# Kernel tuning notes

Measured on AMD Instinct MI355X. Metric: run time of the kernel, lower is better.

Reference implementation:

```python
import jax, jax.numpy as jnp
import numpy as np

T, HID, H, KV, D = 2048, 2048, 16, 8, 128
EPS = 1e-6
THETA = 10000.0


def setup_inputs() -> dict:
    key = jax.random.key(0)
    ks = jax.random.split(key, 4)
    return {
        "positions": jnp.arange(T, dtype=jnp.int32),
        "hidden_states": jax.random.normal(ks[0], (T, HID), dtype=jnp.float32),
        "layernorm_weight": jnp.ones((HID,), dtype=jnp.float32),
        "qkv_weight": jax.random.normal(ks[1], ((H + 2 * KV) * D, HID), dtype=jnp.float32) * 0.02,
        "q_norm_weight": jnp.ones((D,), dtype=jnp.float32),
        "k_norm_weight": jnp.ones((D,), dtype=jnp.float32),
        "o_weight": jax.random.normal(ks[2], (HID, H * D), dtype=jnp.float32) * 0.02,
    }


def _rms(x, w, eps=EPS):
    var = jnp.mean(jnp.square(x), axis=-1, keepdims=True)
    return x * jax.lax.rsqrt(var + eps) * w


def _rope(x, pos):
    # NeoX-style rotary over full head_dim. x: [T, nH, D]
    inv_freq = 1.0 / (THETA ** (jnp.arange(0, D, 2, dtype=jnp.float32) / D))
    ang = pos.astype(jnp.float32)[:, None] * inv_freq  # [T, D/2]
    cos, sin = jnp.cos(ang)[:, None, :], jnp.sin(ang)[:, None, :]
    x1, x2 = x[..., : D // 2], x[..., D // 2 :]
    return jnp.concatenate([x1 * cos - x2 * sin, x2 * cos + x1 * sin], axis=-1)


def reference(positions, hidden_states, layernorm_weight, qkv_weight,
              q_norm_weight, k_norm_weight, o_weight):
    # Fused RMSNorm + QKV projection
    normed = _rms(hidden_states, layernorm_weight)                 # [T, HID]
    qkv = normed @ qkv_weight.T                                    # [T, (H+2KV)*D]
    q, k, v = jnp.split(qkv, [H * D, (H + KV) * D], axis=-1)
    q = _rms(q.reshape(T, H, D), q_norm_weight)                    # per-head q norm
    k = _rms(k.reshape(T, KV, D), k_norm_weight)                   # per-head k norm
    v = v.reshape(T, KV, D)
    # RoPE
    q = _rope(q, positions)
    k = _rope(k, positions)
    # GQA causal attention
    scale = D ** -0.5
    kr = jnp.repeat(k, H // KV, axis=1)                            # [T, H, D]
    vr = jnp.repeat(v, H // KV, axis=1)
    scores = jnp.einsum("qhd,khd->hqk", q, kr) * scale             # [H, T, T]
    mask = jnp.tril(jnp.ones((T, T), dtype=bool))
    scores = jnp.where(mask[None], scores, jnp.finfo(scores.dtype).min)
    attn = jax.nn.softmax(scores, axis=-1)
    out = jnp.einsum("hqk,khd->qhd", attn, vr).reshape(T, H * D)
    return out @ o_weight.T                                        # [T, HID]
```

## Files before the change

kernel.cpp:

```cpp
#include <hip/hip_runtime.h>
#include <cstdint>
#include <cstddef>

typedef __bf16 bf16;
typedef __attribute__((ext_vector_type(8))) __bf16 bf16x8;
typedef __attribute__((ext_vector_type(4))) __bf16 bf16x4v;
typedef __attribute__((ext_vector_type(4))) float f32x4;
typedef __attribute__((ext_vector_type(16))) float f32x16;
typedef __attribute__((ext_vector_type(4))) short short4v;

#define T_N   2048
#define HID_N 2048
#define NH    16
#define NKV   8
#define HD    128

#define MFMA(a, b, c)   __builtin_amdgcn_mfma_f32_16x16x32_bf16((a), (b), (c), 0, 0, 0)
#define MFMA32(a, b, c) __builtin_amdgcn_mfma_f32_32x32x16_bf16((a), (b), (c), 0, 0, 0)

__device__ __forceinline__ f32x4 MFMA16(short4v a, short4v b, f32x4 c) {
#if __has_builtin(__builtin_amdgcn_mfma_f32_16x16x16bf16_1k)
    return __builtin_amdgcn_mfma_f32_16x16x16bf16_1k(a, b, c, 0, 0, 0);
#else
    asm volatile("v_mfma_f32_16x16x16_bf16 %0, %1, %2, %0\n\ts_nop 7\n\ts_nop 7"
                 : "+v"(c) : "v"(a), "v"(b));
    return c;
#endif
}

__device__ __forceinline__ void gl_lds16(const void* g, void* l) {
    __builtin_amdgcn_global_load_lds(
        (const __attribute__((address_space(1))) unsigned int*)g,
        (__attribute__((address_space(3))) unsigned int*)l,
        16, 0, 0);
}

__device__ __forceinline__ uint32_t pk2(float a, float b) {
    union { bf16 h; unsigned short u; } ca, cb;
    ca.h = (bf16)a; cb.h = (bf16)b;
    return ((uint32_t)cb.u << 16) | ca.u;
}

__device__ __forceinline__ void y2cq(int y, int& ci, int& qt) {
    if (y < 25)       { ci = 0; qt = y + 7; }
    else if (y < 42)  { ci = 1; qt = y - 10; }
    else if (y < 51)  { ci = 2; qt = y - 19; }
    else if (y == 51) { ci = 3; qt = 31; }
    else { int z = y - 52; int k = 7 - (z >> 2); ci = z & 3; qt = 8 * ci + k - 1; }
}
__device__ __forceinline__ int yof(int ci, int qt) {
    int k = qt + 1 - 8 * ci;
    if (k >= 8) {
        if (ci == 0) return qt - 7;
        if (ci == 1) return qt + 10;
        if (ci == 2) return qt + 19;
        return 51;
    }
    return 52 + (7 - k) * 4 + ci;
}

__global__ __launch_bounds__(256) void k_pre(const float* __restrict__ qkvw,
                                             bf16* __restrict__ qkvw_b,
                                             const float* __restrict__ ow,
                                             bf16* __restrict__ ow_b,
                                             const float* __restrict__ hid,
                                             const float* __restrict__ lw,
                                             bf16* __restrict__ normed,
                                             const int* __restrict__ pos,
                                             float2* __restrict__ rope) {
    const int blk = blockIdx.x, tid = threadIdx.x;
    if (blk < 6144) {
        const float* src; bf16* dst;
        if (blk < 4096) { int i = blk * 2048 + tid * 8; src = qkvw + i; dst = qkvw_b + i; }
        else            { int i = (blk - 4096) * 2048 + tid * 8; src = ow + i; dst = ow_b + i; }
        float4 x = ((const float4*)src)[0], y = ((const float4*)src)[1];
        bf16x8 v;
        v[0] = (bf16)x.x; v[1] = (bf16)x.y; v[2] = (bf16)x.z; v[3] = (bf16)x.w;
        v[4] = (bf16)y.x; v[5] = (bf16)y.y; v[6] = (bf16)y.z; v[7] = (bf16)y.w;
        *(bf16x8*)dst = v;
        return;
    }
    if (blk >= 8192) {
        const int t = (blk - 8192) * 4 + (tid >> 6);
        const int j = tid & 63;
        float ang = (float)pos[t] * __powf(10000.f, -(float)j * (1.f / 64.f));
        float s, c;
        __sincosf(ang, &s, &c);
        rope[t * 64 + j] = make_float2(c, s);
        return;
    }
    const int row = blk - 6144;
    const float* xr = hid + (size_t)row * HID_N;
    float4 a = ((const float4*)xr)[tid * 2];
    float4 b = ((const float4*)xr)[tid * 2 + 1];
    float ss = a.x*a.x + a.y*a.y + a.z*a.z + a.w*a.w
             + b.x*b.x + b.y*b.y + b.z*b.z + b.w*b.w;
    #pragma unroll
    for (int m = 32; m; m >>= 1) ss += __shfl_xor(ss, m);
    __shared__ float red[4];
    if ((tid & 63) == 0) red[tid >> 6] = ss;
    __syncthreads();
    float tot = red[0] + red[1] + red[2] + red[3];
    float rs = rsqrtf(tot * (1.0f / HID_N) + 1e-6f);
    const float4* wr = (const float4*)(lw + tid * 8);
    float4 wa = wr[0], wb = wr[1];
    bf16x8 v;
    v[0] = (bf16)(a.x * rs * wa.x); v[1] = (bf16)(a.y * rs * wa.y);
    v[2] = (bf16)(a.z * rs * wa.z); v[3] = (bf16)(a.w * rs * wa.w);
    v[4] = (bf16)(b.x * rs * wb.x); v[5] = (bf16)(b.y * rs * wb.y);
    v[6] = (bf16)(b.z * rs * wb.z); v[7] = (bf16)(b.w * rs * wb.w);
    *(bf16x8*)(normed + (size_t)row * HID_N + tid * 8) = v;
}

__global__ __launch_bounds__(256, 3) void k_gemm_qkv(const bf16* __restrict__ A,
                                                     const bf16* __restrict__ B,
                                                     bf16* __restrict__ qkv3,
                                                     bf16* __restrict__ vb) {
    const int K = HID_N;
    __shared__ __attribute__((aligned(16))) bf16 As[128 * 64];
    __shared__ __attribute__((aligned(16))) bf16 Bs[128 * 64];
    const int tid = threadIdx.x;
    const int lane = tid & 63, wid = tid >> 6;
    const int wm = wid >> 1, wn = wid & 1;
    const int col31 = lane & 31, khalf = lane >> 5;
    const int orig = blockIdx.y * gridDim.x + blockIdx.x;
    const int wgid = (orig & 7) * 64 + (orig >> 3);
    const size_t bm = (size_t)(wgid >> 5) * 128, bn = (size_t)(wgid & 31) * 128;

    f32x16 acc[2][2] = {};
    const int srow = tid >> 3;
    const int schk = tid & 7;

    for (int k0 = 0; k0 < K; k0 += 64) {
        __syncthreads();
        #pragma unroll
        for (int c = 0; c < 4; c++) {
            int row = c * 32 + srow;
            int ka = (schk ^ (row & 7)) << 3;
            gl_lds16(A + (bm + row) * (size_t)K + k0 + ka,
                     (char*)As + c * 4096 + tid * 16);
            gl_lds16(B + (bn + row) * (size_t)K + k0 + ka,
                     (char*)Bs + c * 4096 + tid * 16);
        }
        __syncthreads();
        #pragma unroll
        for (int kb = 0; kb < 4; kb++) {
            bf16x8 af[2], bfr[2];
            #pragma unroll
            for (int mt = 0; mt < 2; mt++) {
                int row = wm * 64 + mt * 32 + col31;
                af[mt] = *(const bf16x8*)(As + row * 64 + (((2 * kb + khalf) ^ (row & 7)) << 3));
            }
            #pragma unroll
            for (int nt = 0; nt < 2; nt++) {
                int row = wn * 64 + nt * 32 + col31;
                bfr[nt] = *(const bf16x8*)(Bs + row * 64 + (((2 * kb + khalf) ^ (row & 7)) << 3));
            }
            #pragma unroll
            for (int mt = 0; mt < 2; mt++)
                #pragma unroll
                for (int nt = 0; nt < 2; nt++)
                    acc[mt][nt] = MFMA32(af[mt], bfr[nt], acc[mt][nt]);
        }
    }
    #pragma unroll
    for (int mt = 0; mt < 2; mt++)
        #pragma unroll
        for (int nt = 0; nt < 2; nt++)
            #pragma unroll
            for (int i = 0; i < 16; i++) {
                int rowl = (i & 3) + 8 * (i >> 2) + 4 * khalf;
                size_t row = bm + wm * 64 + mt * 32 + rowl;
                size_t col = bn + wn * 64 + nt * 32 + col31;
                bf16 val = (bf16)acc[mt][nt][i];
                if (col < 3072) qkv3[row * 3072 + col] = val;
                else            vb[row * 1024 + (col - 3072)] = val;
            }
}

__global__ __launch_bounds__(256, 3) void k_gemm_bt64(const bf16* __restrict__ A,
                                                      const bf16* __restrict__ B,
                                                      float* __restrict__ C,
                                                      int M, int N, int K) {
    __shared__ __attribute__((aligned(16))) bf16 As[64 * 64];
    __shared__ __attribute__((aligned(16))) bf16 Bs[128 * 64];
    const int tid = threadIdx.x;
    const int lane = tid & 63, wid = tid >> 6;
    const int col31 = lane & 31, khalf = lane >> 5;
    const int orig = blockIdx.y * gridDim.x + blockIdx.x;
    const int wgid = (orig & 7) * 64 + (orig >> 3);
    const size_t bm = (size_t)(wgid >> 4) * 64, bn = (size_t)(wgid & 15) * 128;

    f32x16 acc[2] = {};
    const int srow = tid >> 3;
    const int schk = tid & 7;

    for (int k0 = 0; k0 < K; k0 += 64) {
        __syncthreads();
        #pragma unroll
        for (int c = 0; c < 2; c++) {
            int row = c * 32 + srow;
            int ka = (schk ^ (row & 7)) << 3;
            gl_lds16(A + (bm + row) * (size_t)K + k0 + ka,
                     (char*)As + c * 4096 + tid * 16);
        }
        #pragma unroll
        for (int c = 0; c < 4; c++) {
            int row = c * 32 + srow;
            int ka = (schk ^ (row & 7)) << 3;
            gl_lds16(B + (bn + row) * (size_t)K + k0 + ka,
                     (char*)Bs + c * 4096 + tid * 16);
        }
        __syncthreads();
        #pragma unroll
        for (int kb = 0; kb < 4; kb++) {
            bf16x8 af[2], bfr;
            #pragma unroll
            for (int mt = 0; mt < 2; mt++) {
                int row = mt * 32 + col31;
                af[mt] = *(const bf16x8*)(As + row * 64 + (((2 * kb + khalf) ^ (row & 7)) << 3));
            }
            {
                int row = wid * 32 + col31;
                bfr = *(const bf16x8*)(Bs + row * 64 + (((2 * kb + khalf) ^ (row & 7)) << 3));
            }
            #pragma unroll
            for (int mt = 0; mt < 2; mt++)
                acc[mt] = MFMA32(af[mt], bfr, acc[mt]);
        }
    }
    #pragma unroll
    for (int mt = 0; mt < 2; mt++)
        #pragma unroll
        for (int i = 0; i < 16; i++) {
            int rowl = (i & 3) + 8 * (i >> 2) + 4 * khalf;
            size_t row = bm + mt * 32 + rowl;
            size_t col = bn + wid * 32 + col31;
            C[row * (size_t)N + col] = acc[mt][i];
        }
}

__global__ __launch_bounds__(256) void k_mid(const bf16* __restrict__ qkv3,
                                             const float* __restrict__ qw,
                                             const float* __restrict__ kw,
                                             const float2* __restrict__ rope,
                                             bf16* __restrict__ q,
                                             bf16* __restrict__ k,
                                             const bf16* __restrict__ vin,
                                             bf16* __restrict__ vT) {
    const int tid = threadIdx.x;
    if (blockIdx.y == 12) {
        const int bx = blockIdx.x;
        if (bx >= 512) return;
        __shared__ bf16 tile[64][72];
        const int tb = bx & 31, db = bx >> 5;
        const int row = tid >> 2, cc = tid & 3;
        const bf16* src = vin + (size_t)(tb * 64 + row) * 1024 + db * 64 + cc * 16;
        bf16x8 a = *(const bf16x8*)(src);
        bf16x8 b = *(const bf16x8*)(src + 8);
        #pragma unroll
        for (int i = 0; i < 8; i++) tile[row][cc * 16 + i] = a[i];
        #pragma unroll
        for (int i = 0; i < 8; i++) tile[row][cc * 16 + 8 + i] = b[i];
        __syncthreads();
        bf16* dst = vT + (size_t)(db * 64 + row) * 2048 + tb * 64 + cc * 16;
        bf16x8 o1, o2;
        #pragma unroll
        for (int i = 0; i < 8; i++) o1[i] = tile[cc * 16 + i][row];
        #pragma unroll
        for (int i = 0; i < 8; i++) o2[i] = tile[cc * 16 + 8 + i][row];
        *(bf16x8*)dst = o1;
        *(bf16x8*)(dst + 8) = o2;
        return;
    }
    const int t = blockIdx.x;
    const int half = tid >> 7, d = tid & 127;
    const int slot = blockIdx.y * 2 + half;
    const bool isq = slot < 16;
    const int h = isq ? slot : slot - 16;
    float x = (float)qkv3[(size_t)t * 3072 + slot * 128 + d];
    float ss = x * x;
    #pragma unroll
    for (int m = 32; m; m >>= 1) ss += __shfl_xor(ss, m);
    __shared__ float red[4];
    __shared__ float sh[256];
    if ((tid & 63) == 0) red[tid >> 6] = ss;
    __syncthreads();
    float rs = rsqrtf((red[half * 2] + red[half * 2 + 1]) * (1.0f / HD) + 1e-6f);
    float nx = x * rs * (isq ? qw[d] : kw[d]);
    sh[tid] = nx;
    __syncthreads();
    float other = sh[tid ^ 64];
    float2 cs = rope[t * 64 + (d & 63)];
    float o = (d < 64) ? (nx * cs.x - other * cs.y) : (nx * cs.x + other * cs.y);
    bf16* dst = isq ? (q + ((size_t)t * NH + h) * HD + d)
                    : (k + ((size_t)t * NKV + h) * HD + d);
    *dst = (bf16)o;
}

__global__ __launch_bounds__(256, 3) void k_flash(const bf16* __restrict__ Q,
                                                  const bf16* __restrict__ K,
                                                  const bf16* __restrict__ VT,
                                                  bf16* __restrict__ On,
                                                  float* __restrict__ ml) {
    __shared__ __attribute__((aligned(16))) bf16 Ks2[2][64 * 128];
    __shared__ __attribute__((aligned(16))) bf16 Vt[128 * 64];

    const int tid = threadIdx.x, lane = tid & 63, w = tid >> 6;
    const int r = lane & 15, g = lane >> 4;
    const int h = blockIdx.x, y = blockIdx.y;
    int ci, qt;
    y2cq(y, ci, qt);
    const int c0 = ci * 8;
    const int ntl = min(qt + 1 - c0, 8);
    const int q0 = qt * 64;
    const int gh = h >> 1;
    const int q0w = q0 + w * 16;

    const int rowk = tid >> 4, posc = tid & 15;
    const int vrow = tid >> 3, vkb = tid & 7;
    const bf16* VTh = VT + (size_t)gh * 128 * 2048;

    bf16x8 qf[4];
    #pragma unroll
    for (int ks = 0; ks < 4; ks++)
        qf[ks] = *(const bf16x8*)(Q + ((size_t)(q0w + r) * NH + h) * HD + ks * 32 + g * 8);

    f32x4 acc[8] = {};
    float m_run = -1e30f, l_run = 0.f;
    const float scale = 0.08838834764831845f;

    {
        const int kv0 = c0 * 64;
        #pragma unroll
        for (int c = 0; c < 4; c++) {
            int row = c * 16 + rowk;
            int srcc = posc ^ (row & 7);
            gl_lds16(K + ((size_t)(kv0 + row) * NKV + gh) * HD + srcc * 8,
                     (char*)&Ks2[0][0] + c * 4096 + tid * 16);
        }
        asm volatile("s_waitcnt vmcnt(0)" ::: "memory");
        __builtin_amdgcn_s_barrier();
    }

    for (int t = 0; t < ntl; ++t) {
        const int b = t & 1;
        const int kv0 = (c0 + t) * 64;
        const bool pf = (t + 1 < ntl);
        #pragma unroll
        for (int it = 0; it < 4; it++) {
            int d = it * 32 + vrow;
            int srck = (vkb ^ (vrow & 7)) * 8;
            gl_lds16(VTh + (size_t)d * 2048 + kv0 + srck,
                     (char*)&Vt[0] + it * 4096 + tid * 16);
        }
        if (pf) {
            const int kv1 = kv0 + 64;
            #pragma unroll
            for (int c = 0; c < 4; c++) {
                int row = c * 16 + rowk;
                int srcc = posc ^ (row & 7);
                gl_lds16(K + ((size_t)(kv1 + row) * NKV + gh) * HD + srcc * 8,
                         (char*)&Ks2[0][0] + (b ^ 1) * 16384 + c * 4096 + tid * 16);
            }
        }
        const bool compute = (kv0 <= q0w + 15);
        union PB { uint32_t u[2]; short4v s; };
        PB pbu[4];
        if (compute) {
            const bf16* Kb = &Ks2[b][0];
            const bool fullt = (kv0 + 63 <= q0w);
            float sc[4][4];
            __builtin_amdgcn_s_setprio(1);
            #pragma unroll
            for (int t4 = 0; t4 < 4; t4++) {
                f32x4 S = {};
                #pragma unroll
                for (int ks = 0; ks < 4; ks++) {
                    int row = t4 * 16 + r;
                    bf16x8 kf = *(const bf16x8*)(Kb + row * 128 + (((4 * ks + g) ^ (row & 7)) * 8));
                    S = MFMA(kf, qf[ks], S);
                }
                if (fullt) {
                    #pragma unroll
                    for (int j = 0; j < 4; j++) sc[t4][j] = S[j] * scale;
                } else {
                    #pragma unroll
                    for (int j = 0; j < 4; j++) {
                        int kg = kv0 + t4 * 16 + 4 * g + j;
                        sc[t4][j] = (kg <= q0w + r) ? S[j] * scale : -1e30f;
                    }
                }
            }
            __builtin_amdgcn_s_setprio(0);
            float mx = sc[0][0];
            #pragma unroll
            for (int t4 = 0; t4 < 4; t4++)
                #pragma unroll
                for (int j = 0; j < 4; j++) mx = fmaxf(mx, sc[t4][j]);
            mx = fmaxf(mx, __shfl_xor(mx, 16));
            mx = fmaxf(mx, __shfl_xor(mx, 32));
            const bool nr = __all(mx <= m_run + 8.0f) != 0;
            float mn, alpha;
            if (nr) { mn = m_run; alpha = 1.0f; }
            else    { mn = fmaxf(m_run, mx); alpha = __expf(m_run - mn); m_run = mn; }
            float rsum = 0.f;
            #pragma unroll
            for (int t4 = 0; t4 < 4; t4++)
                #pragma unroll
                for (int j = 0; j < 4; j++) {
                    sc[t4][j] = __expf(sc[t4][j] - mn);
                    rsum += sc[t4][j];
                }
            rsum += __shfl_xor(rsum, 16);
            rsum += __shfl_xor(rsum, 32);
            l_run = l_run * alpha + rsum;
            if (!nr) {
                #pragma unroll
                for (int f = 0; f < 8; f++)
                    #pragma unroll
                    for (int j = 0; j < 4; j++) acc[f][j] *= alpha;
            }
            #pragma unroll
            for (int t4 = 0; t4 < 4; t4++) {
                pbu[t4].u[0] = pk2(sc[t4][0], sc[t4][1]);
                pbu[t4].u[1] = pk2(sc[t4][2], sc[t4][3]);
            }
        }
        if (pf) asm volatile("s_waitcnt vmcnt(4)" ::: "memory");
        else    asm volatile("s_waitcnt vmcnt(0)" ::: "memory");
        __builtin_amdgcn_s_barrier();
        if (compute) {
            const char* Vb = (const char*)&Vt[0];
            __builtin_amdgcn_s_setprio(1);
            #pragma unroll
            for (int f = 0; f < 8; f++) {
                #pragma unroll
                for (int t4 = 0; t4 < 4; t4++) {
                    short4v vf = *(const short4v*)(Vb + f * 2048 + r * 128 +
                                  (((2 * t4 + (g >> 1)) ^ (r & 7)) * 16) + (g & 1) * 8);
                    acc[f] = MFMA16(vf, pbu[t4].s, acc[f]);
                }
            }
            __builtin_amdgcn_s_setprio(0);
        }
        asm volatile("s_waitcnt vmcnt(0)" ::: "memory");
        __builtin_amdgcn_s_barrier();
    }
    const int lr = w * 16 + r;
    float inv_l = 1.0f / l_run;
    bf16* Ob = On + ((size_t)(h * 80 + y)) * 8192 + lr * 128;
    #pragma unroll
    for (int f = 0; f < 8; f++) {
        bf16x4v ov;
        #pragma unroll
        for (int j = 0; j < 4; j++) ov[j] = (bf16)(acc[f][j] * inv_l);
        *(bf16x4v*)(Ob + f * 16 + 4 * g) = ov;
    }
    if (g == 0) {
        float* mlp = ml + ((size_t)(h * 80 + y)) * 128;
        mlp[lr] = m_run;
        mlp[64 + lr] = l_run;
    }
}

__global__ __launch_bounds__(256) void k_comb(const bf16* __restrict__ On,
                                              const float* __restrict__ ml,
                                              bf16* __restrict__ ao) {
    const int h = blockIdx.x, qt = blockIdx.y;
    const int tid = threadIdx.x;
    const int dc = tid & 15;
    const int qr = tid >> 4;
    const int nc = 1 + (qt >= 8) + (qt >= 16) + (qt >= 24);
    int ys[4];
    #pragma unroll
    for (int i = 0; i < 4; i++) ys[i] = (i < nc) ? yof(i, qt) : 0;
    #pragma unroll
    for (int p = 0; p < 4; p++) {
        const int lq = p * 16 + qr;
        float mi[4], li[4], wi[4];
        float mstar = -1e30f;
        for (int i = 0; i < 4; i++) {
            if (i < nc) {
                const float* pml = ml + ((size_t)(h * 80 + ys[i])) * 128;
                mi[i] = pml[lq]; li[i] = pml[64 + lq];
                mstar = fmaxf(mstar, mi[i]);
            }
        }
        float wsum = 0.f;
        for (int i = 0; i < 4; i++) {
            if (i < nc) { wi[i] = li[i] * __expf(mi[i] - mstar); wsum += wi[i]; }
            else wi[i] = 0.f;
        }
        float inv = 1.f / wsum;
        float o[8] = {};
        for (int i = 0; i < 4; i++) {
            if (i < nc) {
                bf16x8 v = *(const bf16x8*)(On + ((size_t)(h * 80 + ys[i])) * 8192 +
                                            lq * 128 + dc * 8);
                float wn = wi[i] * inv;
                #pragma unroll
                for (int j = 0; j < 8; j++) o[j] += wn * (float)v[j];
            }
        }
        bf16x8 ov;
        #pragma unroll
        for (int j = 0; j < 8; j++) ov[j] = (bf16)o[j];
        const int q = qt * 64 + lq;
        *(bf16x8*)(ao + ((size_t)q * NH + h) * HD + dc * 8) = ov;
    }
}

extern "C" void kernel_launch(void* const* d_in, const int* in_sizes, int n_in,
                              void* d_out, int out_size, void* d_ws, size_t ws_size,
                              hipStream_t stream) {
    const int*   pos  = (const int*)d_in[0];
    const float* hid  = (const float*)d_in[1];
    const float* lw   = (const float*)d_in[2];
    const float* qkvw = (const float*)d_in[3];
    const float* qnw  = (const float*)d_in[4];
    const float* knw  = (const float*)d_in[5];
    const float* ow   = (const float*)d_in[6];
    float* out = (float*)d_out;

    char* ws = (char*)d_ws;
    bf16*   qkvw_b = (bf16*)(ws);
    bf16*   ow_b   = (bf16*)(ws + (16u << 20));
    bf16*   normed = (bf16*)(ws + (24u << 20));
    bf16*   qkv3   = (bf16*)(ws + (32u << 20));
    bf16*   qb     = (bf16*)(ws + (64u << 20));
    bf16*   kb     = (bf16*)(ws + (72u << 20));
    bf16*   vb     = (bf16*)(ws + (76u << 20));
    bf16*   ao     = normed;
    bf16*   On     = (bf16*)(ws + (32u << 20));
    float*  ml     = (float*)(ws + (54u << 20));
    bf16*   vT     = (bf16*)(ws + (56u << 20));
    float2* rope   = (float2*)(ws + (60u << 20));

    k_pre<<<8704, 256, 0, stream>>>(qkvw, qkvw_b, ow, ow_b, hid, lw, normed, pos, rope);
    k_gemm_qkv<<<dim3(32, 16), 256, 0, stream>>>(normed, qkvw_b, qkv3, vb);
    k_mid<<<dim3(T_N, 13), 256, 0, stream>>>(qkv3, qnw, knw, rope, qb, kb, vb, vT);
    k_flash<<<dim3(NH, 80), 256, 0, stream>>>(qb, kb, vT, On, ml);
    k_comb<<<dim3(NH, 32), 256, 0, stream>>>(On, ml, ao);
    k_gemm_bt64<<<dim3(16, 32), 256, 0, stream>>>(ao, ow_b, out, 2048, 2048, 2048);
}
```

Before: 168.6 us.

## Double flash attention query tile to 128 rows with 512-thread blocks

The flash kernel now gives each block a 128-row query tile with 8 waves instead of 64 rows with 4 waves, so each K/V tile staged in LDS serves twice as many queries. The KV-chunk schedule and the combine kernel's index mapping are rewritten to match the halved grid. Global-to-LDS loads per thread drop from 4 to 2, which lowers load traffic per query. In exchange there are fewer blocks (640), bigger per-block causal imbalance, and more wasted masked work on diagonal tiles.

```diff
diff --git a/kernel.cpp b/kernel.cpp
--- a/kernel.cpp
+++ b/kernel.cpp
@@ -41,22 +41,23 @@
     return ((uint32_t)cb.u << 16) | ca.u;
 }
 
-__device__ __forceinline__ void y2cq(int y, int& ci, int& qt) {
-    if (y < 25)       { ci = 0; qt = y + 7; }
-    else if (y < 42)  { ci = 1; qt = y - 10; }
-    else if (y < 51)  { ci = 2; qt = y - 19; }
-    else if (y == 51) { ci = 3; qt = 31; }
-    else { int z = y - 52; int k = 7 - (z >> 2); ci = z & 3; qt = 8 * ci + k - 1; }
-}
-__device__ __forceinline__ int yof(int ci, int qt) {
-    int k = qt + 1 - 8 * ci;
-    if (k >= 8) {
-        if (ci == 0) return qt - 7;
-        if (ci == 1) return qt + 10;
-        if (ci == 2) return qt + 19;
-        return 51;
-    }
-    return 52 + (7 - k) * 4 + ci;
+__device__ __forceinline__ void y2cq2(int y, int& ci, int& qp) {
+    if (y < 13)       { ci = 0; qp = y + 3; }
+    else if (y < 22)  { ci = 1; qp = y - 6; }
+    else if (y < 27)  { ci = 2; qp = y - 11; }
+    else if (y == 27) { ci = 3; qp = 15; }
+    else { int z = y - 28; int ntl = 6 - 2 * (z >> 2); ci = z & 3; qp = ci * 4 + ((ntl - 2) >> 1); }
+}
+__device__ __forceinline__ int yof2(int ci, int qt) {
+    int qp = qt >> 1;
+    if (qp >= 4 * ci + 3) {
+        if (ci == 0) return qp - 3;
+        if (ci == 1) return qp + 6;
+        if (ci == 2) return qp + 11;
+        return 27;
+    }
+    int ntl = 2 * qp + 2 - 8 * ci;
+    return 28 + ((6 - ntl) >> 1) * 4 + ci;
 }
 
 __global__ __launch_bounds__(256) void k_pre(const float* __restrict__ qkvw,
@@ -298,7 +299,7 @@
     *dst = (bf16)o;
 }
 
-__global__ __launch_bounds__(256, 3) void k_flash(const bf16* __restrict__ Q,
+__global__ __launch_bounds__(512, 6) void k_flash(const bf16* __restrict__ Q,
                                                   const bf16* __restrict__ K,
                                                   const bf16* __restrict__ VT,
                                                   bf16* __restrict__ On,
@@ -309,16 +310,15 @@
     const int tid = threadIdx.x, lane = tid & 63, w = tid >> 6;
     const int r = lane & 15, g = lane >> 4;
     const int h = blockIdx.x, y = blockIdx.y;
-    int ci, qt;
-    y2cq(y, ci, qt);
+    int ci, qp;
+    y2cq2(y, ci, qp);
     const int c0 = ci * 8;
-    const int ntl = min(qt + 1 - c0, 8);
-    const int q0 = qt * 64;
+    const int ntl = min(2 * qp + 2 - 8 * ci, 8);
     const int gh = h >> 1;
-    const int q0w = q0 + w * 16;
+    const int q0w = qp * 128 + w * 16;
 
     const int rowk = tid >> 4, posc = tid & 15;
-    const int vrow = tid >> 3, vkb = tid & 7;
+    const int vsub = tid >> 3, vkb = tid & 7;
     const bf16* VTh = VT + (size_t)gh * 128 * 2048;
 
     bf16x8 qf[4];
@@ -333,11 +333,11 @@
     {
         const int kv0 = c0 * 64;
         #pragma unroll
-        for (int c = 0; c < 4; c++) {
-            int row = c * 16 + rowk;
+        for (int c = 0; c < 2; c++) {
+            int row = c * 32 + rowk;
             int srcc = posc ^ (row & 7);
             gl_lds16(K + ((size_t)(kv0 + row) * NKV + gh) * HD + srcc * 8,
-                     (char*)&Ks2[0][0] + c * 4096 + tid * 16);
+                     (char*)&Ks2[0][0] + c * 8192 + tid * 16);
         }
         asm volatile("s_waitcnt vmcnt(0)" ::: "memory");
         __builtin_amdgcn_s_barrier();
@@ -348,20 +348,20 @@
         const int kv0 = (c0 + t) * 64;
         const bool pf = (t + 1 < ntl);
         #pragma unroll
-        for (int it = 0; it < 4; it++) {
-            int d = it * 32 + vrow;
-            int srck = (vkb ^ (vrow & 7)) * 8;
+        for (int it = 0; it < 2; it++) {
+            int d = it * 64 + vsub;
+            int srck = (vkb ^ (vsub & 7)) * 8;
             gl_lds16(VTh + (size_t)d * 2048 + kv0 + srck,
-                     (char*)&Vt[0] + it * 4096 + tid * 16);
+                     (char*)&Vt[0] + it * 8192 + tid * 16);
         }
         if (pf) {
             const int kv1 = kv0 + 64;
             #pragma unroll
-            for (int c = 0; c < 4; c++) {
-                int row = c * 16 + rowk;
+            for (int c = 0; c < 2; c++) {
+                int row = c * 32 + rowk;
                 int srcc = posc ^ (row & 7);
                 gl_lds16(K + ((size_t)(kv1 + row) * NKV + gh) * HD + srcc * 8,
-                         (char*)&Ks2[0][0] + (b ^ 1) * 16384 + c * 4096 + tid * 16);
+                         (char*)&Ks2[0][0] + (b ^ 1) * 16384 + c * 8192 + tid * 16);
             }
         }
         const bool compute = (kv0 <= q0w + 15);
@@ -427,7 +427,7 @@
                 pbu[t4].u[1] = pk2(sc[t4][2], sc[t4][3]);
             }
         }
-        if (pf) asm volatile("s_waitcnt vmcnt(4)" ::: "memory");
+        if (pf) asm volatile("s_waitcnt vmcnt(2)" ::: "memory");
         else    asm volatile("s_waitcnt vmcnt(0)" ::: "memory");
         __builtin_amdgcn_s_barrier();
         if (compute) {
@@ -449,7 +449,7 @@
     }
     const int lr = w * 16 + r;
     float inv_l = 1.0f / l_run;
-    bf16* Ob = On + ((size_t)(h * 80 + y)) * 8192 + lr * 128;
+    bf16* Ob = On + ((size_t)(h * 40 + y)) * 16384 + lr * 128;
     #pragma unroll
     for (int f = 0; f < 8; f++) {
         bf16x4v ov;
@@ -458,9 +458,9 @@
         *(bf16x4v*)(Ob + f * 16 + 4 * g) = ov;
     }
     if (g == 0) {
-        float* mlp = ml + ((size_t)(h * 80 + y)) * 128;
+        float* mlp = ml + ((size_t)(h * 40 + y)) * 256;
         mlp[lr] = m_run;
-        mlp[64 + lr] = l_run;
+        mlp[128 + lr] = l_run;
     }
 }
 
@@ -472,9 +472,10 @@
     const int dc = tid & 15;
     const int qr = tid >> 4;
     const int nc = 1 + (qt >= 8) + (qt >= 16) + (qt >= 24);
+    const int hb = (qt & 1) * 64;
     int ys[4];
     #pragma unroll
-    for (int i = 0; i < 4; i++) ys[i] = (i < nc) ? yof(i, qt) : 0;
+    for (int i = 0; i < 4; i++) ys[i] = (i < nc) ? yof2(i, qt) : 0;
     #pragma unroll
     for (int p = 0; p < 4; p++) {
         const int lq = p * 16 + qr;
@@ -482,8 +483,8 @@
         float mstar = -1e30f;
         for (int i = 0; i < 4; i++) {
             if (i < nc) {
-                const float* pml = ml + ((size_t)(h * 80 + ys[i])) * 128;
-                mi[i] = pml[lq]; li[i] = pml[64 + lq];
+                const float* pml = ml + ((size_t)(h * 40 + ys[i])) * 256;
+                mi[i] = pml[hb + lq]; li[i] = pml[128 + hb + lq];
                 mstar = fmaxf(mstar, mi[i]);
             }
         }
@@ -496,8 +497,8 @@
         float o[8] = {};
         for (int i = 0; i < 4; i++) {
             if (i < nc) {
-                bf16x8 v = *(const bf16x8*)(On + ((size_t)(h * 80 + ys[i])) * 8192 +
-                                            lq * 128 + dc * 8);
+                bf16x8 v = *(const bf16x8*)(On + ((size_t)(h * 40 + ys[i])) * 16384 +
+                                            (hb + lq) * 128 + dc * 8);
                 float wn = wi[i] * inv;
                 #pragma unroll
                 for (int j = 0; j < 8; j++) o[j] += wn * (float)v[j];
@@ -540,7 +541,7 @@
     k_pre<<<8704, 256, 0, stream>>>(qkvw, qkvw_b, ow, ow_b, hid, lw, normed, pos, rope);
     k_gemm_qkv<<<dim3(32, 16), 256, 0, stream>>>(normed, qkvw_b, qkv3, vb);
     k_mid<<<dim3(T_N, 13), 256, 0, stream>>>(qkv3, qnw, knw, rope, qb, kb, vb, vT);
-    k_flash<<<dim3(NH, 80), 256, 0, stream>>>(qb, kb, vT, On, ml);
+    k_flash<<<dim3(NH, 40), 512, 0, stream>>>(qb, kb, vT, On, ml);
     k_comb<<<dim3(NH, 32), 256, 0, stream>>>(On, ml, ao);
     k_gemm_bt64<<<dim3(16, 32), 256, 0, stream>>>(ao, ow_b, out, 2048, 2048, 2048);
 }
```

Result: slower. 207.7 us (+23.2%).
